# Kernel tuning notes

Hardware: AMD Instinct MI355X
Metric: run time of the kernel (lower is better)

The kernel has to match this reference:

```python
import math
import jax, jax.numpy as jnp
import numpy as np

B, C_F, C_A, OUT, L = 32, 128, 128, 128, 8192


def setup_inputs() -> dict:
    key = jax.random.key(0)
    ks = jax.random.split(key, 6)
    x = jax.random.normal(ks[0], (B, C_F, L), dtype=jnp.float32)
    y = jax.random.normal(ks[1], (B, C_A, L), dtype=jnp.float32)
    # torch nn.Linear layout: W (out, in), b (out)
    Wf = jax.random.normal(ks[2], (OUT, C_F), dtype=jnp.float32) / math.sqrt(C_F)
    bf = jax.random.normal(ks[3], (OUT,), dtype=jnp.float32) * 0.02
    Wa = jax.random.normal(ks[4], (OUT, C_A), dtype=jnp.float32) / math.sqrt(C_A)
    ba = jax.random.normal(ks[5], (OUT,), dtype=jnp.float32) * 0.02
    return {"x": x, "y": y, "Wf": Wf, "bf": bf, "Wa": Wa, "ba": ba}


def reference(x, y, Wf, bf, Wa, ba):
    # Project along the channel dim (-2): equivalent to
    # Linear(x.transpose(-2,-1)).transpose(-2,-1) in torch.
    xp = jnp.einsum('bfl,of->bol', x, Wf) + bf[:, None]   # (B, OUT, L)
    yp = jnp.einsum('bal,oa->bol', y, Wa) + ba[:, None]   # (B, OUT, L)
    z = xp + yp                                           # (B, OUT, L)
    d_k = xp.shape[-1]  # = L
    scores = jnp.einsum('bol,bpl->bop', xp, yp)           # (B, OUT, OUT)
    attn = jax.nn.softmax(scores, axis=-1) / jnp.sqrt(jnp.asarray(d_k, xp.dtype))
    out = jnp.einsum('bop,bpl->bol', attn, z)             # (B, OUT, L)
    return out
```

## Files before the change

### kernel.cpp

```cpp
#include <hip/hip_runtime.h>
#include <math.h>

#define NB 32
#define NC 128
#define NL 8192
#define SQRT_L 90.50966799187809f

typedef float f32x4 __attribute__((ext_vector_type(4)));
typedef __bf16 bf16x8 __attribute__((ext_vector_type(8)));

__device__ inline void gload_lds16(const void* g, void* l) {
  __builtin_amdgcn_global_load_lds(
      (const __attribute__((address_space(1))) void*)g,
      (__attribute__((address_space(3))) void*)l, 16, 0, 0);
}

__device__ inline void split8(const float* e, bf16x8& hi, bf16x8& lo) {
#pragma unroll
  for (int j = 0; j < 8; ++j) {
    float f = e[j];
    __bf16 h = (__bf16)f;
    hi[j] = h;
    lo[j] = (__bf16)(f - (float)h);
  }
}

__global__ __launch_bounds__(256, 2) void k_prep(
    const float* __restrict__ Wf, const float* __restrict__ Wa,
    float* __restrict__ zbase, __bf16* __restrict__ ws8)
{
  const int blk = blockIdx.x, t = threadIdx.x;
  if (blk >= 2) {
    f32x4* z = (f32x4*)zbase;
    const int n4 = (NB * NC * NC + 2 * NB * NC) / 4;
    for (int i = (blk - 2) * 256 + t; i < n4; i += 10 * 256) z[i] = (f32x4)0.f;
    return;
  }
  const float* W = blk ? Wa : Wf;
  __bf16* Oh = ws8 + (blk ? 4 : 0) * 16384;
  __bf16* Ol = Oh + 16384;
  __bf16* Th = Ol + 16384;
  __bf16* Tl = Th + 16384;
  __shared__ float lds[NC * NC];
  for (int i = t; i < NC * NC; i += 256) {
    int r = i >> 7, c = i & 127;
    lds[r * 128 + (c ^ (r & 31))] = W[i];
  }
  __syncthreads();
  for (int i = t; i < NC * NC; i += 256) {
    int r = i >> 7, c = i & 127;
    float v = lds[r * 128 + (c ^ (r & 31))];
    __bf16 h = (__bf16)v;
    Oh[i] = h; Ol[i] = (__bf16)(v - (float)h);
    float vt = lds[c * 128 + (r ^ (c & 31))];
    __bf16 ht = (__bf16)vt;
    Th[i] = ht; Tl[i] = (__bf16)(vt - (float)ht);
  }
}

__global__ __launch_bounds__(256, 2) void k_pass1(
    const float* __restrict__ x, const float* __restrict__ y,
    float* __restrict__ G, float* __restrict__ sx, float* __restrict__ sy)
{
  __shared__ float ldsA[2][128 * 32];
  __shared__ float ldsB[2][128 * 32];
  const int b = blockIdx.y;
  const int k0 = blockIdx.x * 512;
  const int tid = threadIdx.x;
  const int wave = tid >> 6, lane = tid & 63;
  const int lr = lane & 15, g = lane >> 4;
  const float* Xb = x + (size_t)b * NC * NL;
  const float* Yb = y + (size_t)b * NC * NL;

  int srow[4], scol[4];
#pragma unroll
  for (int q = 0; q < 4; ++q) {
    int slot = q * 256 + tid;
    int row = slot >> 3, pch = slot & 7;
    srow[q] = row;
    scol[q] = (pch ^ (row & 7)) * 4;
  }

  f32x4 acc[2][8];
#pragma unroll
  for (int t = 0; t < 2; ++t)
#pragma unroll
    for (int n = 0; n < 8; ++n) acc[t][n] = (f32x4)0.f;
  float rsx[2] = {0.f, 0.f};
  float rsy[8] = {0.f, 0.f, 0.f, 0.f, 0.f, 0.f, 0.f, 0.f};

  auto stage = [&](int buf, int s) {
    const int kk = k0 + s * 32;
#pragma unroll
    for (int q = 0; q < 4; ++q)
      gload_lds16(Xb + (size_t)srow[q] * NL + kk + scol[q], &ldsA[buf][(q * 256 + tid) * 4]);
#pragma unroll
    for (int q = 0; q < 4; ++q)
      gload_lds16(Yb + (size_t)srow[q] * NL + kk + scol[q], &ldsB[buf][(q * 256 + tid) * 4]);
  };

  stage(0, 0);
  __syncthreads();

  for (int s = 0; s < 16; ++s) {
    const int cur = s & 1;
    if (s < 15) stage(cur ^ 1, s + 1);

    bf16x8 ah[2], al[2];
#pragma unroll
    for (int t = 0; t < 2; ++t) {
      const int row = wave * 32 + t * 16 + lr;
      const float* base = &ldsA[cur][row * 32];
      f32x4 v0 = *(const f32x4*)(base + ((2 * g) ^ (row & 7)) * 4);
      f32x4 v1 = *(const f32x4*)(base + ((2 * g + 1) ^ (row & 7)) * 4);
      float e[8] = {v0[0], v0[1], v0[2], v0[3], v1[0], v1[1], v1[2], v1[3]};
#pragma unroll
      for (int j = 0; j < 8; ++j) rsx[t] += e[j];
      split8(e, ah[t], al[t]);
    }
#pragma unroll
    for (int n = 0; n < 8; ++n) {
      const int row = n * 16 + lr;
      const float* base = &ldsB[cur][row * 32];
      f32x4 v0 = *(const f32x4*)(base + ((2 * g) ^ (row & 7)) * 4);
      f32x4 v1 = *(const f32x4*)(base + ((2 * g + 1) ^ (row & 7)) * 4);
      float e[8] = {v0[0], v0[1], v0[2], v0[3], v1[0], v1[1], v1[2], v1[3]};
      if (wave == 0) {
#pragma unroll
        for (int j = 0; j < 8; ++j) rsy[n] += e[j];
      }
      bf16x8 bh, bl;
      split8(e, bh, bl);
#pragma unroll
      for (int t = 0; t < 2; ++t) {
        acc[t][n] = __builtin_amdgcn_mfma_f32_16x16x32_bf16(ah[t], bh, acc[t][n], 0, 0, 0);
        acc[t][n] = __builtin_amdgcn_mfma_f32_16x16x32_bf16(ah[t], bl, acc[t][n], 0, 0, 0);
        acc[t][n] = __builtin_amdgcn_mfma_f32_16x16x32_bf16(al[t], bh, acc[t][n], 0, 0, 0);
      }
    }
    __syncthreads();
  }

  float* Gb = G + (size_t)b * NC * NC;
#pragma unroll
  for (int t = 0; t < 2; ++t)
#pragma unroll
    for (int n = 0; n < 8; ++n)
#pragma unroll
      for (int r = 0; r < 4; ++r) {
        const int row = wave * 32 + t * 16 + g * 4 + r;
        const int col = n * 16 + lr;
        atomicAdd(&Gb[row * NC + col], acc[t][n][r]);
      }
#pragma unroll
  for (int t = 0; t < 2; ++t) {
    float v = rsx[t];
    v += __shfl_xor(v, 16);
    v += __shfl_xor(v, 32);
    if (lane < 16) atomicAdd(&sx[b * NC + wave * 32 + t * 16 + lr], v);
  }
  if (wave == 0) {
#pragma unroll
    for (int n = 0; n < 8; ++n) {
      float v = rsy[n];
      v += __shfl_xor(v, 16);
      v += __shfl_xor(v, 32);
      if (lane < 16) atomicAdd(&sy[b * NC + n * 16 + lr], v);
    }
  }
}

__global__ __launch_bounds__(256, 2) void k_p2(
    const float* __restrict__ G, const __bf16* __restrict__ ws8,
    const float* __restrict__ Wf, const float* __restrict__ Wa,
    const float* __restrict__ bfv, const float* __restrict__ bav,
    const float* __restrict__ sx, const float* __restrict__ sy,
    float* __restrict__ uv, __bf16* __restrict__ AhO, __bf16* __restrict__ AlO,
    float* __restrict__ cvec)
{
  __shared__ __bf16 sH[NC * NC];
  __shared__ __bf16 sL[NC * NC];
  const __bf16* Wf_h = ws8;
  const __bf16* Wf_l = ws8 + 16384;
  const __bf16* WfT_h = ws8 + 2 * 16384;
  const __bf16* WfT_l = ws8 + 3 * 16384;
  const __bf16* Wa_h = ws8 + 4 * 16384;
  const __bf16* Wa_l = ws8 + 5 * 16384;
  const __bf16* WaT_h = ws8 + 6 * 16384;
  const __bf16* WaT_l = ws8 + 7 * 16384;

  const int b = blockIdx.x;
  const int tid = threadIdx.x;
  const int wave = tid >> 6, lane = tid & 63;
  const int lr = lane & 15, g = lane >> 4;
  const int strip = wave * 32;

  {
    const int o = tid & 127;
    const float* Wrow = (tid < 128 ? Wf : Wa) + o * NC;
    const float* sv = (tid < 128 ? sx : sy) + b * NC;
    const f32x4* W4 = (const f32x4*)Wrow;
    const f32x4* S4 = (const f32x4*)sv;
    float a = 0.f;
#pragma unroll
    for (int f4 = 0; f4 < 32; ++f4) {
      f32x4 w = W4[f4], s = S4[f4];
      a += w[0] * s[0] + w[1] * s[1] + w[2] * s[2] + w[3] * s[3];
    }
    uv[b * 256 + tid] = a;
  }

  const float* Gb = G + (size_t)b * NC * NC;

  {
    f32x4 a1[2][8];
#pragma unroll
    for (int t = 0; t < 2; ++t)
#pragma unroll
      for (int n = 0; n < 8; ++n) a1[t][n] = (f32x4)0.f;
#pragma unroll
    for (int ks = 0; ks < 4; ++ks) {
      const int a0 = ks * 32 + g * 8;
      bf16x8 wh[2], wl[2];
#pragma unroll
      for (int t = 0; t < 2; ++t) {
        const int p = strip + t * 16 + lr;
        wh[t] = *(const bf16x8*)(Wa_h + p * NC + a0);
        wl[t] = *(const bf16x8*)(Wa_l + p * NC + a0);
      }
#pragma unroll
      for (int n = 0; n < 8; ++n) {
        const int f = n * 16 + lr;
        f32x4 g0 = *(const f32x4*)(Gb + (size_t)f * NC + a0);
        f32x4 g1 = *(const f32x4*)(Gb + (size_t)f * NC + a0 + 4);
        float e[8] = {g0[0], g0[1], g0[2], g0[3], g1[0], g1[1], g1[2], g1[3]};
        bf16x8 gh, gl;
        split8(e, gh, gl);
#pragma unroll
        for (int t = 0; t < 2; ++t) {
          a1[t][n] = __builtin_amdgcn_mfma_f32_16x16x32_bf16(wh[t], gh, a1[t][n], 0, 0, 0);
          a1[t][n] = __builtin_amdgcn_mfma_f32_16x16x32_bf16(wh[t], gl, a1[t][n], 0, 0, 0);
          a1[t][n] = __builtin_amdgcn_mfma_f32_16x16x32_bf16(wl[t], gh, a1[t][n], 0, 0, 0);
        }
      }
    }
#pragma unroll
    for (int t = 0; t < 2; ++t)
#pragma unroll
      for (int n = 0; n < 8; ++n)
#pragma unroll
        for (int r = 0; r < 4; ++r) {
          const int p = strip + t * 16 + g * 4 + r;
          const int f = n * 16 + lr;
          const int idx = p * 128 + ((((f >> 3)) ^ (p & 7)) << 3) + (f & 7);
          float v = a1[t][n][r];
          __bf16 h = (__bf16)v;
          sH[idx] = h;
          sL[idx] = (__bf16)(v - (float)h);
        }
  }
  __syncthreads();

  f32x4 s2[2][8];
#pragma unroll
  for (int t = 0; t < 2; ++t)
#pragma unroll
    for (int n = 0; n < 8; ++n) s2[t][n] = (f32x4)0.f;
#pragma unroll
  for (int ks = 0; ks < 4; ++ks) {
    const int f0 = ks * 32 + g * 8;
    const int chunk = ks * 4 + g;
    bf16x8 wh[2], wl[2];
#pragma unroll
    for (int t = 0; t < 2; ++t) {
      const int o = strip + t * 16 + lr;
      wh[t] = *(const bf16x8*)(Wf_h + o * NC + f0);
      wl[t] = *(const bf16x8*)(Wf_l + o * NC + f0);
    }
#pragma unroll
    for (int n = 0; n < 8; ++n) {
      const int p = n * 16 + lr;
      const int idx = p * 128 + ((chunk ^ (p & 7)) << 3);
      bf16x8 mh = *(const bf16x8*)&sH[idx];
      bf16x8 ml = *(const bf16x8*)&sL[idx];
#pragma unroll
      for (int t = 0; t < 2; ++t) {
        s2[t][n] = __builtin_amdgcn_mfma_f32_16x16x32_bf16(wh[t], mh, s2[t][n], 0, 0, 0);
        s2[t][n] = __builtin_amdgcn_mfma_f32_16x16x32_bf16(wh[t], ml, s2[t][n], 0, 0, 0);
        s2[t][n] = __builtin_amdgcn_mfma_f32_16x16x32_bf16(wl[t], mh, s2[t][n], 0, 0, 0);
      }
    }
  }

  float u_r[2][4], bf_r[2][4], v_c[8], ba_c[8], bb_c[8];
#pragma unroll
  for (int t = 0; t < 2; ++t)
#pragma unroll
    for (int r = 0; r < 4; ++r) {
      const int row = strip + t * 16 + g * 4 + r;
      u_r[t][r] = uv[b * 256 + row];
      bf_r[t][r] = bfv[row];
    }
#pragma unroll
  for (int n = 0; n < 8; ++n) {
    const int p = n * 16 + lr;
    v_c[n] = uv[b * 256 + 128 + p];
    ba_c[n] = bav[p];
    bb_c[n] = bfv[p] + bav[p];
  }
#pragma unroll
  for (int t = 0; t < 2; ++t)
#pragma unroll
    for (int n = 0; n < 8; ++n)
#pragma unroll
      for (int r = 0; r < 4; ++r)
        s2[t][n][r] += u_r[t][r] * ba_c[n] + bf_r[t][r] * (v_c[n] + 8192.0f * ba_c[n]);

  float cd[2][4];
#pragma unroll
  for (int t = 0; t < 2; ++t)
#pragma unroll
    for (int r = 0; r < 4; ++r) {
      float m = -3.4e38f;
#pragma unroll
      for (int n = 0; n < 8; ++n) m = fmaxf(m, s2[t][n][r]);
      m = fmaxf(m, __shfl_xor(m, 1));
      m = fmaxf(m, __shfl_xor(m, 2));
      m = fmaxf(m, __shfl_xor(m, 4));
      m = fmaxf(m, __shfl_xor(m, 8));
      float e[8], sum = 0.f;
#pragma unroll
      for (int n = 0; n < 8; ++n) { e[n] = __expf(s2[t][n][r] - m); sum += e[n]; }
      sum += __shfl_xor(sum, 1);
      sum += __shfl_xor(sum, 2);
      sum += __shfl_xor(sum, 4);
      sum += __shfl_xor(sum, 8);
      const float inv = 1.f / (sum * SQRT_L);
      float c = 0.f;
#pragma unroll
      for (int n = 0; n < 8; ++n) { float a = e[n] * inv; s2[t][n][r] = a; c += a * bb_c[n]; }
      c += __shfl_xor(c, 1);
      c += __shfl_xor(c, 2);
      c += __shfl_xor(c, 4);
      c += __shfl_xor(c, 8);
      cd[t][r] = c;
    }
  if (lr == 0) {
#pragma unroll
    for (int t = 0; t < 2; ++t)
#pragma unroll
      for (int r = 0; r < 4; ++r)
        cvec[b * NC + strip + t * 16 + g * 4 + r] = cd[t][r];
  }
  __syncthreads();

#pragma unroll
  for (int t = 0; t < 2; ++t)
#pragma unroll
    for (int n = 0; n < 8; ++n)
#pragma unroll
      for (int r = 0; r < 4; ++r) {
        const int o = strip + t * 16 + g * 4 + r;
        const int p = n * 16 + lr;
        const int idx = o * 128 + ((((p >> 3)) ^ (o & 7)) << 3) + (p & 7);
        float a = s2[t][n][r];
        __bf16 h = (__bf16)a;
        sH[idx] = h;
        sL[idx] = (__bf16)(a - (float)h);
      }
  __syncthreads();

#pragma unroll
  for (int half = 0; half < 2; ++half) {
    const __bf16* Bh = half ? WaT_h : WfT_h;
    const __bf16* Bl = half ? WaT_l : WfT_l;
    f32x4 a3[2][8];
#pragma unroll
    for (int t = 0; t < 2; ++t)
#pragma unroll
      for (int n = 0; n < 8; ++n) a3[t][n] = (f32x4)0.f;
#pragma unroll
    for (int ks = 0; ks < 4; ++ks) {
      const int p0 = ks * 32 + g * 8;
      const int chunk = ks * 4 + g;
      bf16x8 th[2], tl[2];
#pragma unroll
      for (int t = 0; t < 2; ++t) {
        const int o = strip + t * 16 + lr;
        const int idx = o * 128 + ((chunk ^ (o & 7)) << 3);
        th[t] = *(const bf16x8*)&sH[idx];
        tl[t] = *(const bf16x8*)&sL[idx];
      }
#pragma unroll
      for (int n = 0; n < 8; ++n) {
        const int c = n * 16 + lr;
        bf16x8 bh = *(const bf16x8*)(Bh + c * NC + p0);
        bf16x8 bl = *(const bf16x8*)(Bl + c * NC + p0);
#pragma unroll
        for (int t = 0; t < 2; ++t) {
          a3[t][n] = __builtin_amdgcn_mfma_f32_16x16x32_bf16(th[t], bh, a3[t][n], 0, 0, 0);
          a3[t][n] = __builtin_amdgcn_mfma_f32_16x16x32_bf16(th[t], bl, a3[t][n], 0, 0, 0);
          a3[t][n] = __builtin_amdgcn_mfma_f32_16x16x32_bf16(tl[t], bh, a3[t][n], 0, 0, 0);
        }
      }
    }
#pragma unroll
    for (int t = 0; t < 2; ++t)
#pragma unroll
      for (int n = 0; n < 8; ++n)
#pragma unroll
        for (int r = 0; r < 4; ++r) {
          const int o = strip + t * 16 + g * 4 + r;
          const int c = half * 128 + n * 16 + lr;
          const size_t off = ((size_t)(b * NC + o)) * 256 + c;
          float v = a3[t][n][r];
          __bf16 h = (__bf16)v;
          AhO[off] = h;
          AlO[off] = (__bf16)(v - (float)h);
        }
  }
}

__global__ __launch_bounds__(512, 4) void k_pass3(
    const float* __restrict__ x, const float* __restrict__ y,
    const __bf16* __restrict__ Ah, const __bf16* __restrict__ Al,
    const float* __restrict__ cvec, float* __restrict__ out)
{
  __shared__ float sS[2][32 * 128];
  const int b = blockIdx.y;
  const int l0 = blockIdx.x * 128;
  const int tid = threadIdx.x;
  const int wave = tid >> 6, lane = tid & 63;
  const int lr = lane & 15, g = lane >> 4;
  const int mg = wave >> 1, ch = wave & 1;

  int sk[2], sc[2];
#pragma unroll
  for (int q = 0; q < 2; ++q) {
    int slot = q * 512 + tid;
    int k = slot >> 5, pch = slot & 31;
    int gr = (k >> 3) & 3;
    sk[q] = k;
    sc[q] = ((pch - 2 * gr) & 31) * 4;
  }

  f32x4 acc[2][4];
#pragma unroll
  for (int t = 0; t < 2; ++t)
#pragma unroll
    for (int nt = 0; nt < 4; ++nt) acc[t][nt] = (f32x4)0.f;

  auto stage = [&](int buf, int s) {
    const float* S = (s < 4 ? x : y) + (size_t)b * NC * NL;
    const int chan0 = (s & 3) * 32;
#pragma unroll
    for (int q = 0; q < 2; ++q)
      gload_lds16(S + (size_t)(chan0 + sk[q]) * NL + l0 + sc[q],
                  &sS[buf][(q * 512 + tid) * 4]);
  };

  stage(0, 0);
  __syncthreads();

  for (int s = 0; s < 8; ++s) {
    const int cur = s & 1;
    if (s < 7) stage(cur ^ 1, s + 1);

    bf16x8 a_h[2], a_l[2];
#pragma unroll
    for (int t = 0; t < 2; ++t) {
      const size_t off = ((size_t)(b * NC + mg * 32 + t * 16 + lr)) * 256 + s * 32 + g * 8;
      a_h[t] = *(const bf16x8*)(Ah + off);
      a_l[t] = *(const bf16x8*)(Al + off);
    }
#pragma unroll
    for (int nt = 0; nt < 4; ++nt) {
      const int col = ch * 64 + nt * 16 + lr;
      const int base = ((((col >> 2) + 2 * g) & 31) << 2) + (col & 3);
      float e[8];
#pragma unroll
      for (int j = 0; j < 8; ++j) e[j] = sS[cur][(g * 8 + j) * 128 + base];
      bf16x8 bh, bl;
      split8(e, bh, bl);
#pragma unroll
      for (int t = 0; t < 2; ++t) {
        acc[t][nt] = __builtin_amdgcn_mfma_f32_16x16x32_bf16(a_h[t], bh, acc[t][nt], 0, 0, 0);
        acc[t][nt] = __builtin_amdgcn_mfma_f32_16x16x32_bf16(a_h[t], bl, acc[t][nt], 0, 0, 0);
        acc[t][nt] = __builtin_amdgcn_mfma_f32_16x16x32_bf16(a_l[t], bh, acc[t][nt], 0, 0, 0);
      }
    }
    __syncthreads();
  }

  float* outb = out + (size_t)b * NC * NL;
#pragma unroll
  for (int t = 0; t < 2; ++t)
#pragma unroll
    for (int r = 0; r < 4; ++r) {
      const int row = mg * 32 + t * 16 + g * 4 + r;
      const float cv = cvec[b * NC + row];
#pragma unroll
      for (int nt = 0; nt < 4; ++nt)
        outb[(size_t)row * NL + l0 + ch * 64 + nt * 16 + lr] = acc[t][nt][r] + cv;
    }
}

extern "C" void kernel_launch(void* const* d_in, const int* in_sizes, int n_in,
                              void* d_out, int out_size, void* d_ws, size_t ws_size,
                              hipStream_t stream)
{
  const float* x = (const float*)d_in[0];
  const float* y = (const float*)d_in[1];
  const float* Wf = (const float*)d_in[2];
  const float* bfv = (const float*)d_in[3];
  const float* Wa = (const float*)d_in[4];
  const float* bav = (const float*)d_in[5];
  float* out = (float*)d_out;

  float* G = (float*)d_ws;
  float* sx = G + (size_t)NB * NC * NC;
  float* sy = sx + NB * NC;
  float* uv = sy + NB * NC;
  float* cv = uv + NB * 256;
  __bf16* ws8 = (__bf16*)(cv + NB * NC);
  __bf16* Ah = ws8 + 8 * 16384;
  __bf16* Al = Ah + (size_t)NB * NC * 256;

  k_prep<<<12, 256, 0, stream>>>(Wf, Wa, G, ws8);
  k_pass1<<<dim3(16, NB), 256, 0, stream>>>(x, y, G, sx, sy);
  k_p2<<<NB, 256, 0, stream>>>(G, ws8, Wf, Wa, bfv, bav, sx, sy, uv, Ah, Al, cv);
  k_pass3<<<dim3(NL / 128, NB), 512, 0, stream>>>(x, y, Ah, Al, cv, out);
}
```

Baseline: 502.1 us.

## Deepen LDS prefetch pipelines, widen pass1 blocks, split p2 across rows, stage A via LDS

Pass1 moves to 512-thread blocks with one 16-row strip per wave and a two-stage-ahead async LDS pipeline driven by explicit vmcnt waits, raw barriers and setprio around the MFMA loop. k_p2 now runs 4 blocks per batch, each handling 32 output rows, with the softmax done through an LDS score tile. The A matrix is stored interleaved hi/lo in 64-element chunks so pass3 can stream it into LDS with global_load_lds alongside x/y tiles. The goal is better latency hiding and parallelism in p2, in exchange for more LDS use and hand-tuned wait counts that must match the number of loads in flight.

```diff
diff --git a/kernel.cpp b/kernel.cpp
--- a/kernel.cpp
+++ b/kernel.cpp
@@ -8,6 +8,8 @@
 
 typedef float f32x4 __attribute__((ext_vector_type(4)));
 typedef __bf16 bf16x8 __attribute__((ext_vector_type(8)));
+
+#define BAR() __builtin_amdgcn_s_barrier()
 
 __device__ inline void gload_lds16(const void* g, void* l) {
   __builtin_amdgcn_global_load_lds(
@@ -58,7 +60,7 @@
   }
 }
 
-__global__ __launch_bounds__(256, 2) void k_pass1(
+__global__ __launch_bounds__(512, 2) void k_pass1(
     const float* __restrict__ x, const float* __restrict__ y,
     float* __restrict__ G, float* __restrict__ sx, float* __restrict__ sy)
 {
@@ -72,52 +74,52 @@
   const float* Xb = x + (size_t)b * NC * NL;
   const float* Yb = y + (size_t)b * NC * NL;
 
-  int srow[4], scol[4];
-#pragma unroll
-  for (int q = 0; q < 4; ++q) {
-    int slot = q * 256 + tid;
+  int srow[2], scol[2];
+#pragma unroll
+  for (int q = 0; q < 2; ++q) {
+    int slot = q * 512 + tid;
     int row = slot >> 3, pch = slot & 7;
     srow[q] = row;
     scol[q] = (pch ^ (row & 7)) * 4;
   }
 
-  f32x4 acc[2][8];
-#pragma unroll
-  for (int t = 0; t < 2; ++t)
-#pragma unroll
-    for (int n = 0; n < 8; ++n) acc[t][n] = (f32x4)0.f;
-  float rsx[2] = {0.f, 0.f};
+  f32x4 acc[8];
+#pragma unroll
+  for (int n = 0; n < 8; ++n) acc[n] = (f32x4)0.f;
+  float rsx = 0.f;
   float rsy[8] = {0.f, 0.f, 0.f, 0.f, 0.f, 0.f, 0.f, 0.f};
 
   auto stage = [&](int buf, int s) {
     const int kk = k0 + s * 32;
 #pragma unroll
-    for (int q = 0; q < 4; ++q)
-      gload_lds16(Xb + (size_t)srow[q] * NL + kk + scol[q], &ldsA[buf][(q * 256 + tid) * 4]);
-#pragma unroll
-    for (int q = 0; q < 4; ++q)
-      gload_lds16(Yb + (size_t)srow[q] * NL + kk + scol[q], &ldsB[buf][(q * 256 + tid) * 4]);
+    for (int q = 0; q < 2; ++q)
+      gload_lds16(Xb + (size_t)srow[q] * NL + kk + scol[q], &ldsA[buf][(q * 512 + tid) * 4]);
+#pragma unroll
+    for (int q = 0; q < 2; ++q)
+      gload_lds16(Yb + (size_t)srow[q] * NL + kk + scol[q], &ldsB[buf][(q * 512 + tid) * 4]);
   };
 
   stage(0, 0);
-  __syncthreads();
+  stage(1, 1);
 
   for (int s = 0; s < 16; ++s) {
     const int cur = s & 1;
-    if (s < 15) stage(cur ^ 1, s + 1);
-
-    bf16x8 ah[2], al[2];
-#pragma unroll
-    for (int t = 0; t < 2; ++t) {
-      const int row = wave * 32 + t * 16 + lr;
+    if (s < 15) { asm volatile("s_waitcnt vmcnt(4)" ::: "memory"); }
+    else        { asm volatile("s_waitcnt vmcnt(0)" ::: "memory"); }
+    BAR();
+
+    bf16x8 ah, al;
+    {
+      const int row = wave * 16 + lr;
       const float* base = &ldsA[cur][row * 32];
       f32x4 v0 = *(const f32x4*)(base + ((2 * g) ^ (row & 7)) * 4);
       f32x4 v1 = *(const f32x4*)(base + ((2 * g + 1) ^ (row & 7)) * 4);
       float e[8] = {v0[0], v0[1], v0[2], v0[3], v1[0], v1[1], v1[2], v1[3]};
 #pragma unroll
-      for (int j = 0; j < 8; ++j) rsx[t] += e[j];
-      split8(e, ah[t], al[t]);
-    }
+      for (int j = 0; j < 8; ++j) rsx += e[j];
+      split8(e, ah, al);
+    }
+    __builtin_amdgcn_s_setprio(1);
 #pragma unroll
     for (int n = 0; n < 8; ++n) {
       const int row = n * 16 + lr;
@@ -131,33 +133,30 @@
       }
       bf16x8 bh, bl;
       split8(e, bh, bl);
-#pragma unroll
-      for (int t = 0; t < 2; ++t) {
-        acc[t][n] = __builtin_amdgcn_mfma_f32_16x16x32_bf16(ah[t], bh, acc[t][n], 0, 0, 0);
-        acc[t][n] = __builtin_amdgcn_mfma_f32_16x16x32_bf16(ah[t], bl, acc[t][n], 0, 0, 0);
-        acc[t][n] = __builtin_amdgcn_mfma_f32_16x16x32_bf16(al[t], bh, acc[t][n], 0, 0, 0);
-      }
-    }
-    __syncthreads();
+      acc[n] = __builtin_amdgcn_mfma_f32_16x16x32_bf16(ah, bh, acc[n], 0, 0, 0);
+      acc[n] = __builtin_amdgcn_mfma_f32_16x16x32_bf16(ah, bl, acc[n], 0, 0, 0);
+      acc[n] = __builtin_amdgcn_mfma_f32_16x16x32_bf16(al, bh, acc[n], 0, 0, 0);
+    }
+    __builtin_amdgcn_s_setprio(0);
+    asm volatile("s_waitcnt lgkmcnt(0)" ::: "memory");
+    BAR();
+    if (s < 14) stage(cur, s + 2);
   }
 
   float* Gb = G + (size_t)b * NC * NC;
 #pragma unroll
-  for (int t = 0; t < 2; ++t)
-#pragma unroll
-    for (int n = 0; n < 8; ++n)
-#pragma unroll
-      for (int r = 0; r < 4; ++r) {
-        const int row = wave * 32 + t * 16 + g * 4 + r;
-        const int col = n * 16 + lr;
-        atomicAdd(&Gb[row * NC + col], acc[t][n][r]);
-      }
-#pragma unroll
-  for (int t = 0; t < 2; ++t) {
-    float v = rsx[t];
+  for (int n = 0; n < 8; ++n)
+#pragma unroll
+    for (int r = 0; r < 4; ++r) {
+      const int row = wave * 16 + g * 4 + r;
+      const int col = n * 16 + lr;
+      atomicAdd(&Gb[row * NC + col], acc[n][r]);
+    }
+  {
+    float v = rsx;
     v += __shfl_xor(v, 16);
     v += __shfl_xor(v, 32);
-    if (lane < 16) atomicAdd(&sx[b * NC + wave * 32 + t * 16 + lr], v);
+    if (lane < 16) atomicAdd(&sx[b * NC + wave * 16 + lr], v);
   }
   if (wave == 0) {
 #pragma unroll
@@ -175,11 +174,14 @@
     const float* __restrict__ Wf, const float* __restrict__ Wa,
     const float* __restrict__ bfv, const float* __restrict__ bav,
     const float* __restrict__ sx, const float* __restrict__ sy,
-    float* __restrict__ uv, __bf16* __restrict__ AhO, __bf16* __restrict__ AlO,
-    float* __restrict__ cvec)
+    __bf16* __restrict__ Aout, float* __restrict__ cvec)
 {
-  __shared__ __bf16 sH[NC * NC];
-  __shared__ __bf16 sL[NC * NC];
+  __shared__ __bf16 sMtH[NC * NC];
+  __shared__ __bf16 sMtL[NC * NC];
+  __shared__ float sSc[32 * 128];
+  __shared__ float su[32];
+  __shared__ float sv[128];
+
   const __bf16* Wf_h = ws8;
   const __bf16* Wf_l = ws8 + 16384;
   const __bf16* WfT_h = ws8 + 2 * 16384;
@@ -189,25 +191,33 @@
   const __bf16* WaT_h = ws8 + 6 * 16384;
   const __bf16* WaT_l = ws8 + 7 * 16384;
 
-  const int b = blockIdx.x;
+  const int b = blockIdx.y;
+  const int so0 = blockIdx.x * 32;
   const int tid = threadIdx.x;
   const int wave = tid >> 6, lane = tid & 63;
   const int lr = lane & 15, g = lane >> 4;
-  const int strip = wave * 32;
-
-  {
-    const int o = tid & 127;
-    const float* Wrow = (tid < 128 ? Wf : Wa) + o * NC;
-    const float* sv = (tid < 128 ? sx : sy) + b * NC;
-    const f32x4* W4 = (const f32x4*)Wrow;
-    const f32x4* S4 = (const f32x4*)sv;
+
+  if (tid < 32) {
+    const f32x4* W4 = (const f32x4*)(Wf + (size_t)(so0 + tid) * NC);
+    const f32x4* S4 = (const f32x4*)(sx + b * NC);
     float a = 0.f;
 #pragma unroll
-    for (int f4 = 0; f4 < 32; ++f4) {
-      f32x4 w = W4[f4], s = S4[f4];
+    for (int i = 0; i < 32; ++i) {
+      f32x4 w = W4[i], s = S4[i];
       a += w[0] * s[0] + w[1] * s[1] + w[2] * s[2] + w[3] * s[3];
     }
-    uv[b * 256 + tid] = a;
+    su[tid] = a;
+  } else if (tid >= 128) {
+    const int p = tid - 128;
+    const f32x4* W4 = (const f32x4*)(Wa + (size_t)p * NC);
+    const f32x4* S4 = (const f32x4*)(sy + b * NC);
+    float a = 0.f;
+#pragma unroll
+    for (int i = 0; i < 32; ++i) {
+      f32x4 w = W4[i], s = S4[i];
+      a += w[0] * s[0] + w[1] * s[1] + w[2] * s[2] + w[3] * s[3];
+    }
+    sv[p] = a;
   }
 
   const float* Gb = G + (size_t)b * NC * NC;
@@ -224,7 +234,7 @@
       bf16x8 wh[2], wl[2];
 #pragma unroll
       for (int t = 0; t < 2; ++t) {
-        const int p = strip + t * 16 + lr;
+        const int p = wave * 32 + t * 16 + lr;
         wh[t] = *(const bf16x8*)(Wa_h + p * NC + a0);
         wl[t] = *(const bf16x8*)(Wa_l + p * NC + a0);
       }
@@ -250,22 +260,22 @@
       for (int n = 0; n < 8; ++n)
 #pragma unroll
         for (int r = 0; r < 4; ++r) {
-          const int p = strip + t * 16 + g * 4 + r;
+          const int p = wave * 32 + t * 16 + g * 4 + r;
           const int f = n * 16 + lr;
-          const int idx = p * 128 + ((((f >> 3)) ^ (p & 7)) << 3) + (f & 7);
+          const int idx = p * 128 + (((f >> 3) ^ (p & 7)) << 3) + (f & 7);
           float v = a1[t][n][r];
           __bf16 h = (__bf16)v;
-          sH[idx] = h;
-          sL[idx] = (__bf16)(v - (float)h);
+          sMtH[idx] = h;
+          sMtL[idx] = (__bf16)(v - (float)h);
         }
   }
   __syncthreads();
 
-  f32x4 s2[2][8];
+  f32x4 s2[2][2];
 #pragma unroll
   for (int t = 0; t < 2; ++t)
 #pragma unroll
-    for (int n = 0; n < 8; ++n) s2[t][n] = (f32x4)0.f;
+    for (int n = 0; n < 2; ++n) s2[t][n] = (f32x4)0.f;
 #pragma unroll
   for (int ks = 0; ks < 4; ++ks) {
     const int f0 = ks * 32 + g * 8;
@@ -273,16 +283,16 @@
     bf16x8 wh[2], wl[2];
 #pragma unroll
     for (int t = 0; t < 2; ++t) {
-      const int o = strip + t * 16 + lr;
+      const int o = so0 + t * 16 + lr;
       wh[t] = *(const bf16x8*)(Wf_h + o * NC + f0);
       wl[t] = *(const bf16x8*)(Wf_l + o * NC + f0);
     }
 #pragma unroll
-    for (int n = 0; n < 8; ++n) {
-      const int p = n * 16 + lr;
+    for (int n = 0; n < 2; ++n) {
+      const int p = (wave * 2 + n) * 16 + lr;
       const int idx = p * 128 + ((chunk ^ (p & 7)) << 3);
-      bf16x8 mh = *(const bf16x8*)&sH[idx];
-      bf16x8 ml = *(const bf16x8*)&sL[idx];
+      bf16x8 mh = *(const bf16x8*)&sMtH[idx];
+      bf16x8 ml = *(const bf16x8*)&sMtL[idx];
 #pragma unroll
       for (int t = 0; t < 2; ++t) {
         s2[t][n] = __builtin_amdgcn_mfma_f32_16x16x32_bf16(wh[t], mh, s2[t][n], 0, 0, 0);
@@ -291,94 +301,72 @@
       }
     }
   }
-
-  float u_r[2][4], bf_r[2][4], v_c[8], ba_c[8], bb_c[8];
-#pragma unroll
-  for (int t = 0; t < 2; ++t)
-#pragma unroll
-    for (int r = 0; r < 4; ++r) {
-      const int row = strip + t * 16 + g * 4 + r;
-      u_r[t][r] = uv[b * 256 + row];
-      bf_r[t][r] = bfv[row];
-    }
-#pragma unroll
-  for (int n = 0; n < 8; ++n) {
-    const int p = n * 16 + lr;
-    v_c[n] = uv[b * 256 + 128 + p];
-    ba_c[n] = bav[p];
-    bb_c[n] = bfv[p] + bav[p];
-  }
-#pragma unroll
-  for (int t = 0; t < 2; ++t)
-#pragma unroll
-    for (int n = 0; n < 8; ++n)
-#pragma unroll
-      for (int r = 0; r < 4; ++r)
-        s2[t][n][r] += u_r[t][r] * ba_c[n] + bf_r[t][r] * (v_c[n] + 8192.0f * ba_c[n]);
-
-  float cd[2][4];
-#pragma unroll
-  for (int t = 0; t < 2; ++t)
-#pragma unroll
-    for (int r = 0; r < 4; ++r) {
-      float m = -3.4e38f;
-#pragma unroll
-      for (int n = 0; n < 8; ++n) m = fmaxf(m, s2[t][n][r]);
-      m = fmaxf(m, __shfl_xor(m, 1));
-      m = fmaxf(m, __shfl_xor(m, 2));
-      m = fmaxf(m, __shfl_xor(m, 4));
-      m = fmaxf(m, __shfl_xor(m, 8));
-      float e[8], sum = 0.f;
-#pragma unroll
-      for (int n = 0; n < 8; ++n) { e[n] = __expf(s2[t][n][r] - m); sum += e[n]; }
-      sum += __shfl_xor(sum, 1);
-      sum += __shfl_xor(sum, 2);
-      sum += __shfl_xor(sum, 4);
-      sum += __shfl_xor(sum, 8);
-      const float inv = 1.f / (sum * SQRT_L);
-      float c = 0.f;
-#pragma unroll
-      for (int n = 0; n < 8; ++n) { float a = e[n] * inv; s2[t][n][r] = a; c += a * bb_c[n]; }
-      c += __shfl_xor(c, 1);
-      c += __shfl_xor(c, 2);
-      c += __shfl_xor(c, 4);
-      c += __shfl_xor(c, 8);
-      cd[t][r] = c;
-    }
-  if (lr == 0) {
+  __syncthreads();
+
+#pragma unroll
+  for (int n = 0; n < 2; ++n) {
+    const int p = (wave * 2 + n) * 16 + lr;
+    const float bap = bav[p];
+    const float svp = sv[p] + 8192.0f * bap;
 #pragma unroll
     for (int t = 0; t < 2; ++t)
 #pragma unroll
-      for (int r = 0; r < 4; ++r)
-        cvec[b * NC + strip + t * 16 + g * 4 + r] = cd[t][r];
+      for (int r = 0; r < 4; ++r) {
+        const int o_ = t * 16 + g * 4 + r;
+        sSc[o_ * 128 + p] = s2[t][n][r] + su[o_] * bap + bfv[so0 + o_] * svp;
+      }
   }
   __syncthreads();
 
-#pragma unroll
-  for (int t = 0; t < 2; ++t)
-#pragma unroll
-    for (int n = 0; n < 8; ++n)
-#pragma unroll
-      for (int r = 0; r < 4; ++r) {
-        const int o = strip + t * 16 + g * 4 + r;
-        const int p = n * 16 + lr;
-        const int idx = o * 128 + ((((p >> 3)) ^ (o & 7)) << 3) + (p & 7);
-        float a = s2[t][n][r];
-        __bf16 h = (__bf16)a;
-        sH[idx] = h;
-        sL[idx] = (__bf16)(a - (float)h);
-      }
+  {
+    const int row = tid >> 3, j = tid & 7;
+    const float* sr = &sSc[row * 128 + j * 16];
+    float m = -3.4e38f;
+#pragma unroll
+    for (int i = 0; i < 16; ++i) m = fmaxf(m, sr[i]);
+    m = fmaxf(m, __shfl_xor(m, 1));
+    m = fmaxf(m, __shfl_xor(m, 2));
+    m = fmaxf(m, __shfl_xor(m, 4));
+    float e[16], sum = 0.f;
+#pragma unroll
+    for (int i = 0; i < 16; ++i) { e[i] = __expf(sr[i] - m); sum += e[i]; }
+    sum += __shfl_xor(sum, 1);
+    sum += __shfl_xor(sum, 2);
+    sum += __shfl_xor(sum, 4);
+    const float inv = 1.f / (sum * SQRT_L);
+    float c = 0.f;
+    bf16x8 hv[2], lv[2];
+#pragma unroll
+    for (int i = 0; i < 16; ++i) {
+      const int p = j * 16 + i;
+      float a = e[i] * inv;
+      c += a * (bfv[p] + bav[p]);
+      __bf16 h = (__bf16)a;
+      hv[i >> 3][i & 7] = h;
+      lv[i >> 3][i & 7] = (__bf16)(a - (float)h);
+    }
+#pragma unroll
+    for (int q = 0; q < 2; ++q) {
+      const int chunk = (j * 2 + q) ^ (row & 15);
+      *(bf16x8*)&sMtH[row * 128 + chunk * 8] = hv[q];
+      *(bf16x8*)&sMtL[row * 128 + chunk * 8] = lv[q];
+    }
+    c += __shfl_xor(c, 1);
+    c += __shfl_xor(c, 2);
+    c += __shfl_xor(c, 4);
+    if (j == 0) cvec[b * NC + so0 + row] = c;
+  }
   __syncthreads();
 
 #pragma unroll
   for (int half = 0; half < 2; ++half) {
     const __bf16* Bh = half ? WaT_h : WfT_h;
     const __bf16* Bl = half ? WaT_l : WfT_l;
-    f32x4 a3[2][8];
+    f32x4 a3[2][2];
 #pragma unroll
     for (int t = 0; t < 2; ++t)
 #pragma unroll
-      for (int n = 0; n < 8; ++n) a3[t][n] = (f32x4)0.f;
+      for (int n = 0; n < 2; ++n) a3[t][n] = (f32x4)0.f;
 #pragma unroll
     for (int ks = 0; ks < 4; ++ks) {
       const int p0 = ks * 32 + g * 8;
@@ -386,16 +374,16 @@
       bf16x8 th[2], tl[2];
 #pragma unroll
       for (int t = 0; t < 2; ++t) {
-        const int o = strip + t * 16 + lr;
-        const int idx = o * 128 + ((chunk ^ (o & 7)) << 3);
-        th[t] = *(const bf16x8*)&sH[idx];
-        tl[t] = *(const bf16x8*)&sL[idx];
-      }
-#pragma unroll
-      for (int n = 0; n < 8; ++n) {
-        const int c = n * 16 + lr;
-        bf16x8 bh = *(const bf16x8*)(Bh + c * NC + p0);
-        bf16x8 bl = *(const bf16x8*)(Bl + c * NC + p0);
+        const int o_ = t * 16 + lr;
+        const int idx = o_ * 128 + ((chunk ^ (o_ & 15)) << 3);
+        th[t] = *(const bf16x8*)&sMtH[idx];
+        tl[t] = *(const bf16x8*)&sMtL[idx];
+      }
+#pragma unroll
+      for (int n = 0; n < 2; ++n) {
+        const int cc = (wave * 2 + n) * 16 + lr;
+        bf16x8 bh = *(const bf16x8*)(Bh + cc * NC + p0);
+        bf16x8 bl = *(const bf16x8*)(Bl + cc * NC + p0);
 #pragma unroll
         for (int t = 0; t < 2; ++t) {
           a3[t][n] = __builtin_amdgcn_mfma_f32_16x16x32_bf16(th[t], bh, a3[t][n], 0, 0, 0);
@@ -407,26 +395,27 @@
 #pragma unroll
     for (int t = 0; t < 2; ++t)
 #pragma unroll
-      for (int n = 0; n < 8; ++n)
+      for (int n = 0; n < 2; ++n)
 #pragma unroll
         for (int r = 0; r < 4; ++r) {
-          const int o = strip + t * 16 + g * 4 + r;
-          const int c = half * 128 + n * 16 + lr;
-          const size_t off = ((size_t)(b * NC + o)) * 256 + c;
+          const int o = so0 + t * 16 + g * 4 + r;
+          const int cg = half * 128 + (wave * 2 + n) * 16 + lr;
+          const size_t base = ((size_t)(b * 128 + o) * 8 + (cg >> 5)) * 64 + (cg & 31);
           float v = a3[t][n][r];
           __bf16 h = (__bf16)v;
-          AhO[off] = h;
-          AlO[off] = (__bf16)(v - (float)h);
+          Aout[base] = h;
+          Aout[base + 32] = (__bf16)(v - (float)h);
         }
   }
 }
 
 __global__ __launch_bounds__(512, 4) void k_pass3(
     const float* __restrict__ x, const float* __restrict__ y,
-    const __bf16* __restrict__ Ah, const __bf16* __restrict__ Al,
-    const float* __restrict__ cvec, float* __restrict__ out)
+    const __bf16* __restrict__ A, const float* __restrict__ cvec,
+    float* __restrict__ out)
 {
   __shared__ float sS[2][32 * 128];
+  __shared__ __bf16 sA[2][128 * 64];
   const int b = blockIdx.y;
   const int l0 = blockIdx.x * 128;
   const int tid = threadIdx.x;
@@ -443,6 +432,14 @@
     sk[q] = k;
     sc[q] = ((pch - 2 * gr) & 31) * 4;
   }
+  int ar[2], ac[2];
+#pragma unroll
+  for (int q = 0; q < 2; ++q) {
+    int slot = q * 512 + tid;
+    int row = slot >> 3, pch = slot & 7;
+    ar[q] = row;
+    ac[q] = (pch ^ (row & 7)) * 8;
+  }
 
   f32x4 acc[2][4];
 #pragma unroll
@@ -457,22 +454,30 @@
     for (int q = 0; q < 2; ++q)
       gload_lds16(S + (size_t)(chan0 + sk[q]) * NL + l0 + sc[q],
                   &sS[buf][(q * 512 + tid) * 4]);
+#pragma unroll
+    for (int q = 0; q < 2; ++q)
+      gload_lds16(A + ((size_t)(b * 128 + ar[q]) * 8 + s) * 64 + ac[q],
+                  &sA[buf][(q * 512 + tid) * 8]);
   };
 
   stage(0, 0);
-  __syncthreads();
+  stage(1, 1);
 
   for (int s = 0; s < 8; ++s) {
     const int cur = s & 1;
-    if (s < 7) stage(cur ^ 1, s + 1);
+    if (s < 7) { asm volatile("s_waitcnt vmcnt(4)" ::: "memory"); }
+    else       { asm volatile("s_waitcnt vmcnt(0)" ::: "memory"); }
+    BAR();
 
     bf16x8 a_h[2], a_l[2];
 #pragma unroll
     for (int t = 0; t < 2; ++t) {
-      const size_t off = ((size_t)(b * NC + mg * 32 + t * 16 + lr)) * 256 + s * 32 + g * 8;
-      a_h[t] = *(const bf16x8*)(Ah + off);
-      a_l[t] = *(const bf16x8*)(Al + off);
-    }
+      const int row = mg * 32 + t * 16 + lr;
+      const __bf16* base = &sA[cur][row * 64];
+      a_h[t] = *(const bf16x8*)(base + (g ^ (row & 7)) * 8);
+      a_l[t] = *(const bf16x8*)(base + ((4 | g) ^ (row & 7)) * 8);
+    }
+    __builtin_amdgcn_s_setprio(1);
 #pragma unroll
     for (int nt = 0; nt < 4; ++nt) {
       const int col = ch * 64 + nt * 16 + lr;
@@ -489,7 +494,10 @@
         acc[t][nt] = __builtin_amdgcn_mfma_f32_16x16x32_bf16(a_l[t], bh, acc[t][nt], 0, 0, 0);
       }
     }
-    __syncthreads();
+    __builtin_amdgcn_s_setprio(0);
+    asm volatile("s_waitcnt lgkmcnt(0)" ::: "memory");
+    BAR();
+    if (s < 6) stage(cur, s + 2);
   }
 
   float* outb = out + (size_t)b * NC * NL;
@@ -520,14 +528,12 @@
   float* G = (float*)d_ws;
   float* sx = G + (size_t)NB * NC * NC;
   float* sy = sx + NB * NC;
-  float* uv = sy + NB * NC;
-  float* cv = uv + NB * 256;
+  float* cv = sy + NB * NC;
   __bf16* ws8 = (__bf16*)(cv + NB * NC);
-  __bf16* Ah = ws8 + 8 * 16384;
-  __bf16* Al = Ah + (size_t)NB * NC * 256;
+  __bf16* Aout = ws8 + 8 * 16384;
 
   k_prep<<<12, 256, 0, stream>>>(Wf, Wa, G, ws8);
-  k_pass1<<<dim3(16, NB), 256, 0, stream>>>(x, y, G, sx, sy);
-  k_p2<<<NB, 256, 0, stream>>>(G, ws8, Wf, Wa, bfv, bav, sx, sy, uv, Ah, Al, cv);
-  k_pass3<<<dim3(NL / 128, NB), 512, 0, stream>>>(x, y, Ah, Al, cv, out);
-}
+  k_pass1<<<dim3(16, NB), 512, 0, stream>>>(x, y, G, sx, sy);
+  k_p2<<<dim3(4, NB), 256, 0, stream>>>(G, ws8, Wf, Wa, bfv, bav, sx, sy, Aout, cv);
+  k_pass3<<<dim3(NL / 128, NB), 512, 0, stream>>>(x, y, Aout, cv, out);
+}
```

Measured after the change: 449.1 us. -10.6%, faster.
